# Kernel tuning notes

Hardware: AMD Instinct MI355X
Metric: run time of the kernel (lower is better)

Reference implementation:

```python
import jax, jax.numpy as jnp
import numpy as np

EMB = 1024
HEADS = 16
EPS = 1e-6


def setup_inputs() -> dict:
    key = jax.random.key(0)
    ks = jax.random.split(key, 12)
    B, S, D = 2, 2048, EMB
    scale = 1.0 / np.sqrt(D)
    inp = {
        "v": jax.random.normal(ks[0], (B, S, D), jnp.float32),
        "k": jax.random.normal(ks[1], (B, S, D), jnp.float32),
        "q": jax.random.normal(ks[2], (B, S, D), jnp.float32),
        "Wv": jax.random.normal(ks[3], (D, D), jnp.float32) * scale,
        "bv": jnp.zeros((D,), jnp.float32),
        "Wk": jax.random.normal(ks[4], (D, D), jnp.float32) * scale,
        "bk": jnp.zeros((D,), jnp.float32),
        "Wq": jax.random.normal(ks[5], (D, D), jnp.float32) * scale,
        "bq": jnp.zeros((D,), jnp.float32),
        "Wo": jax.random.normal(ks[6], (D, D), jnp.float32) * scale,
        "bo": jnp.zeros((D,), jnp.float32),
        "gamma": jnp.ones((D,), jnp.float32),
        "beta": jnp.zeros((D,), jnp.float32),
    }
    return inp


def reference(v, k, q, Wv, bv, Wk, bk, Wq, bq, Wo, bo, gamma, beta):
    B, S, D = q.shape
    H = HEADS
    d = D // H  # head depth

    def split_heads(x):  # [B,S,D] -> [B,H,S,d]
        return x.reshape(B, S, H, d).transpose(0, 2, 1, 3)

    V = split_heads(v @ Wv + bv)
    K = split_heads(k @ Wk + bk)
    Q = split_heads(q @ Wq + bq)

    # scaled dot-product attention (full score matrix, no mask)
    scores = jnp.einsum("bhqd,bhkd->bhqk", Q, K) / jnp.sqrt(jnp.float32(d))
    attn = jax.nn.softmax(scores, axis=-1)
    ctx = jnp.einsum("bhqk,bhkd->bhqd", attn, V)

    ctx = ctx.transpose(0, 2, 1, 3).reshape(B, S, D)
    out = ctx @ Wo + bo + q  # final dense + residual

    # LayerNormalization(epsilon=1e-6) over last axis
    mu = jnp.mean(out, axis=-1, keepdims=True)
    var = jnp.var(out, axis=-1, keepdims=True)
    return gamma * (out - mu) * jax.lax.rsqrt(var + EPS) + beta
```

## Files before the change

kernel.cpp:

```cpp
#include <hip/hip_runtime.h>
#include <hip/hip_bf16.h>
#include <math.h>

#define D_EMB 1024
#define NBATCH 2
#define SEQ 2048
#define NH 16
#define HDIM 64
#define MTOT (NBATCH*SEQ)
#define NT (SEQ/64)

typedef unsigned short u16;
typedef __attribute__((ext_vector_type(8))) short bf16x8;
typedef __attribute__((ext_vector_type(4))) float f32x4;
typedef __attribute__((ext_vector_type(16))) float f32x16;
typedef __attribute__((ext_vector_type(4))) unsigned short u16x4;
typedef __attribute__((ext_vector_type(4))) unsigned int u32x4;

__device__ __forceinline__ u16 f2b(float f) {
  union { float f; unsigned u; } x; x.f = f;
  unsigned r = x.u + 0x7fffu + ((x.u >> 16) & 1u);
  return (u16)(r >> 16);
}
__device__ __forceinline__ float b2f(u16 u) {
  union { unsigned u; float f; } x; x.u = ((unsigned)u) << 16;
  return x.f;
}

__device__ __forceinline__ void gld_lds16(const u16* g, u16* l) {
  __builtin_amdgcn_global_load_lds(
      (const __attribute__((address_space(1))) void*)g,
      (__attribute__((address_space(3))) void*)l, 16, 0, 0);
}

__global__ __launch_bounds__(256) void convert_qkv(
    const float* __restrict__ v, const float* __restrict__ k, const float* __restrict__ q,
    u16* __restrict__ vb, u16* __restrict__ kb, u16* __restrict__ qb) {
  int idx = blockIdx.x * 256 + threadIdx.x;
  float4 a;
  u16x4 o;
  a = ((const float4*)v)[idx];
  o.x = f2b(a.x); o.y = f2b(a.y); o.z = f2b(a.z); o.w = f2b(a.w);
  ((u16x4*)vb)[idx] = o;
  a = ((const float4*)k)[idx];
  o.x = f2b(a.x); o.y = f2b(a.y); o.z = f2b(a.z); o.w = f2b(a.w);
  ((u16x4*)kb)[idx] = o;
  a = ((const float4*)q)[idx];
  o.x = f2b(a.x); o.y = f2b(a.y); o.z = f2b(a.z); o.w = f2b(a.w);
  ((u16x4*)qb)[idx] = o;
}

__global__ __launch_bounds__(256) void transpose_w(
    const float* __restrict__ Wv, const float* __restrict__ Wk,
    const float* __restrict__ Wq, const float* __restrict__ Wo,
    u16* __restrict__ Wvt, u16* __restrict__ Wkt,
    u16* __restrict__ Wqt, u16* __restrict__ Wot) {
  __shared__ float tile[32][33];
  int z = blockIdx.z;
  const float* W = (z==0) ? Wv : (z==1) ? Wk : (z==2) ? Wq : Wo;
  u16* Wt = (z==0) ? Wvt : (z==1) ? Wkt : (z==2) ? Wqt : Wot;
  int tx = threadIdx.x, ty = threadIdx.y;
  int n0 = blockIdx.x * 32, k0 = blockIdx.y * 32;
#pragma unroll
  for (int i = 0; i < 4; ++i)
    tile[ty + i*8][tx] = W[(size_t)(k0 + ty + i*8) * D_EMB + n0 + tx];
  __syncthreads();
#pragma unroll
  for (int i = 0; i < 4; ++i)
    Wt[(size_t)(n0 + ty + i*8) * D_EMB + k0 + tx] = f2b(tile[tx][ty + i*8]);
}

__global__ __launch_bounds__(256) void transpose_v(
    const u16* __restrict__ Vh, u16* __restrict__ Vt) {
  __shared__ u16 t[64][65];
  const int bhx = blockIdx.y, s0 = blockIdx.x * 64;
  const int tid = threadIdx.x;
  const u16* src = Vh + ((size_t)bhx * SEQ + s0) * HDIM;
  const int r = tid >> 3, seg = (tid & 7) * 8;
  bf16x8 a0 = *(const bf16x8*)(src + (size_t)r * HDIM + seg);
  bf16x8 a1 = *(const bf16x8*)(src + (size_t)(r + 32) * HDIM + seg);
#pragma unroll
  for (int j = 0; j < 8; ++j) {
    t[r][seg + j] = (u16)a0[j];
    t[r + 32][seg + j] = (u16)a1[j];
  }
  __syncthreads();
  const int dd = tid >> 3, ss = (tid & 7) * 8;
  bf16x8 w0, w1;
#pragma unroll
  for (int j = 0; j < 8; ++j) {
    w0[j] = (short)t[ss + j][dd];
    w1[j] = (short)t[ss + j][dd + 32];
  }
  *(bf16x8*)(Vt + ((size_t)bhx * HDIM + dd) * SEQ + s0 + ss) = w0;
  *(bf16x8*)(Vt + ((size_t)bhx * HDIM + dd + 32) * SEQ + s0 + ss) = w1;
}

__device__ __forceinline__ void gemm_loop64(
    const u16* __restrict__ A, const u16* __restrict__ Bt,
    u16* lds_a, u16* lds_b, int bm, int bn, int wid, int lane,
    f32x4 acc[4][2]) {
#pragma unroll 1
  for (int kt = 0; kt < D_EMB/64; ++kt) {
    __syncthreads();
#pragma unroll
    for (int i = 0; i < 2; ++i) {
      int chunk = wid*2 + i;
      int row = chunk*8 + (lane >> 3);
      int slot = (lane & 7) ^ (row & 7);
      gld_lds16(A + (size_t)(bm*64 + row) * D_EMB + kt*64 + slot*8,
                lds_a + chunk*512);
    }
#pragma unroll
    for (int i = 0; i < 4; ++i) {
      int chunk = i*4 + wid;
      int row = chunk*8 + (lane >> 3);
      int slot = (lane & 7) ^ (row & 7);
      gld_lds16(Bt + (size_t)(bn*128 + row) * D_EMB + kt*64 + slot*8,
                lds_b + chunk*512);
    }
    __syncthreads();
#pragma unroll
    for (int st = 0; st < 2; ++st) {
      bf16x8 af[4], bfr[2];
#pragma unroll
      for (int mb = 0; mb < 4; ++mb) {
        int row = mb*16 + (lane & 15);
        int slot = (st*4 + (lane >> 4)) ^ (row & 7);
        af[mb] = *(const bf16x8*)(lds_a + row*64 + slot*8);
      }
#pragma unroll
      for (int nb = 0; nb < 2; ++nb) {
        int row = wid*32 + nb*16 + (lane & 15);
        int slot = (st*4 + (lane >> 4)) ^ (row & 7);
        bfr[nb] = *(const bf16x8*)(lds_b + row*64 + slot*8);
      }
#pragma unroll
      for (int mb = 0; mb < 4; ++mb)
#pragma unroll
        for (int nb = 0; nb < 2; ++nb)
          acc[mb][nb] = __builtin_amdgcn_mfma_f32_16x16x32_bf16(af[mb], bfr[nb], acc[mb][nb], 0, 0, 0);
    }
  }
}

__global__ __launch_bounds__(256) void gemm_qkv(
    const u16* __restrict__ vb, const u16* __restrict__ kb, const u16* __restrict__ qb,
    const u16* __restrict__ Wvt, const u16* __restrict__ Wkt, const u16* __restrict__ Wqt,
    const float* __restrict__ bv, const float* __restrict__ bk, const float* __restrict__ bq,
    u16* __restrict__ Vh, u16* __restrict__ Kh, u16* __restrict__ Qh) {
  __shared__ u16 lds_a[64*64];
  __shared__ u16 lds_b[128*64];
  int z = blockIdx.z;
  const u16* A  = (z==0) ? vb : (z==1) ? kb : qb;
  const u16* Bt = (z==0) ? Wvt : (z==1) ? Wkt : Wqt;
  const float* bias = (z==0) ? bv : (z==1) ? bk : bq;
  u16* Out = (z==0) ? Vh : (z==1) ? Kh : Qh;
  int tid = threadIdx.x, wid = tid >> 6, lane = tid & 63;
  int bm = blockIdx.y, bn = blockIdx.x;
  f32x4 acc[4][2];
#pragma unroll
  for (int i = 0; i < 4; ++i)
#pragma unroll
    for (int j = 0; j < 2; ++j) acc[i][j] = (f32x4){0.f,0.f,0.f,0.f};
  gemm_loop64(A, Bt, lds_a, lds_b, bm, bn, wid, lane, acc);
  int g = lane >> 4, c = lane & 15;
  const float scl = (z == 2) ? 0.18033688f : 1.0f;
#pragma unroll
  for (int mb = 0; mb < 4; ++mb) {
    int row0 = bm*64 + mb*16 + g*4;
#pragma unroll
    for (int nb = 0; nb < 2; ++nb) {
      int col = bn*128 + wid*32 + nb*16 + c;
      float bsv = bias[col];
      int h = col >> 6, dd = col & 63;
#pragma unroll
      for (int r = 0; r < 4; ++r) {
        int m = row0 + r; int b = m >> 11, s = m & (SEQ-1);
        Out[(((size_t)b*NH + h)*SEQ + s)*HDIM + dd] = f2b((acc[mb][nb][r] + bsv) * scl);
      }
    }
  }
}

__global__ __launch_bounds__(256, 2) void attn_k(
    const u16* __restrict__ Qh, const u16* __restrict__ Kh,
    const u16* __restrict__ Vt, u16* __restrict__ ctx) {
  __shared__ u16 kt_lds[2][64*64];
  __shared__ u16 vt_lds[2][64*64];
  const int tid = threadIdx.x, wid = tid >> 6, lane = tid & 63;
  const int lo5 = lane & 31, hi = lane >> 5;
  const int bid = blockIdx.x;
  const int xcd = bid & 7, idx = bid >> 3;
  const int qblk = idx & 15, bhg = idx >> 4;
  const int bh = bhg * 8 + xcd;
  const int qb = qblk * 128 + wid * 32;
  const size_t base = (size_t)bh * SEQ * HDIM;

  const int srow = tid >> 3;
  const int c0 = (tid & 7) ^ (srow & 7) ^ (srow >> 3);
  const int c1 = c0 ^ 4;
  const u16* kp0 = Kh + base + (size_t)srow * HDIM + c0*8;
  const u16* kp1 = Kh + base + (size_t)(srow+32) * HDIM + c1*8;
  const u16* vp0 = Vt + base + (size_t)srow * SEQ + c0*8;
  const u16* vp1 = Vt + base + (size_t)(srow+32) * SEQ + c1*8;

  const int r7 = lo5 & 7, r3 = lo5 >> 3;
  int offs0[4], offs1[4];
#pragma unroll
  for (int t = 0; t < 4; ++t) {
    int p = (2*t + hi) ^ r7 ^ r3;
    offs0[t] = lo5*128 + p*16;
    offs1[t] = (lo5+32)*128 + (p^4)*16;
  }
  const char* ktbase = (const char*)&kt_lds[0][0];
  const char* vtbase = (const char*)&vt_lds[0][0];

  bf16x8 qf[4];
#pragma unroll
  for (int t = 0; t < 4; ++t)
    qf[t] = *(const bf16x8*)(Qh + base + (size_t)(qb + lo5)*HDIM + t*16 + hi*8);

  f32x16 z16;
#pragma unroll
  for (int i = 0; i < 16; ++i) z16[i] = 0.f;

  f32x16 o0, o1;
#pragma unroll
  for (int i = 0; i < 16; ++i) { o0[i] = 0.f; o1[i] = 0.f; }
  float lsum = 0.f;

#define STAGE(B) do { \
    gld_lds16(kp0, &kt_lds[B][wid*512]); \
    gld_lds16(kp1, &kt_lds[B][2048 + wid*512]); \
    gld_lds16(vp0, &vt_lds[B][wid*512]); \
    gld_lds16(vp1, &vt_lds[B][2048 + wid*512]); \
    kp0 += 64*HDIM; kp1 += 64*HDIM; vp0 += 64; vp1 += 64; \
  } while (0)

#define TILE(B, VMSTR, DOSTAGE) do { \
    asm volatile("s_waitcnt " VMSTR ::: "memory"); \
    __builtin_amdgcn_sched_barrier(0); \
    __builtin_amdgcn_s_barrier();             \
    __builtin_amdgcn_sched_barrier(0); \
    const char* kb_ = ktbase + (B)*8192; \
    const char* vb_ = vtbase + (B)*8192; \
    bf16x8 kf0[4], kf1[4], vf0[4], vf1[4]; \
    _Pragma("unroll") for (int t = 0; t < 4; ++t) { \
      kf0[t] = *(const bf16x8*)(kb_ + offs0[t]); \
      kf1[t] = *(const bf16x8*)(kb_ + offs1[t]); \
      vf0[t] = *(const bf16x8*)(vb_ + offs0[t]); \
      vf1[t] = *(const bf16x8*)(vb_ + offs1[t]); } \
    asm volatile("s_waitcnt lgkmcnt(0)" ::: "memory"); \
    __builtin_amdgcn_sched_barrier(0); \
    __builtin_amdgcn_s_barrier();             \
    __builtin_amdgcn_sched_barrier(0); \
    if (DOSTAGE) { STAGE(B); } \
    __builtin_amdgcn_sched_barrier(0); \
    __builtin_amdgcn_s_setprio(1); \
    f32x16 st0 = __builtin_amdgcn_mfma_f32_32x32x16_bf16(kf0[0], qf[0], z16, 0, 0, 0); \
    f32x16 st1 = __builtin_amdgcn_mfma_f32_32x32x16_bf16(kf1[0], qf[0], z16, 0, 0, 0); \
    _Pragma("unroll") for (int t = 1; t < 4; ++t) { \
      st0 = __builtin_amdgcn_mfma_f32_32x32x16_bf16(kf0[t], qf[t], st0, 0, 0, 0); \
      st1 = __builtin_amdgcn_mfma_f32_32x32x16_bf16(kf1[t], qf[t], st1, 0, 0, 0); } \
    __builtin_amdgcn_s_setprio(0); \
    _Pragma("unroll") for (int r = 0; r < 16; ++r) { \
      st0[r] = exp2f(st0[r]); st1[r] = exp2f(st1[r]); } \
    float ps = st0[0] + st0[1]; \
    _Pragma("unroll") for (int r = 2; r < 16; ++r) ps += st0[r]; \
    _Pragma("unroll") for (int r = 0; r < 16; ++r) ps += st1[r]; \
    lsum += ps; \
    bf16x8 pa[4]; \
    _Pragma("unroll") for (int ks = 0; ks < 2; ++ks) { \
      const f32x16& s_ = ks ? st1 : st0; \
      unsigned X[8]; \
      _Pragma("unroll") for (int w = 0; w < 8; ++w) { \
        float lo_f = s_[2*w], hi_f = s_[2*w + 1]; \
        asm("v_cvt_pk_bf16_f32 %0, %1, %2" : "=v"(X[w]) : "v"(lo_f), "v"(hi_f)); } \
      asm volatile("v_permlane32_swap_b32 %0, %1" : "+v"(X[0]), "+v"(X[2])); \
      asm volatile("v_permlane32_swap_b32 %0, %1" : "+v"(X[1]), "+v"(X[3])); \
      asm volatile("v_permlane32_swap_b32 %0, %1" : "+v"(X[4]), "+v"(X[6])); \
      asm volatile("v_permlane32_swap_b32 %0, %1" : "+v"(X[5]), "+v"(X[7])); \
      union { u32x4 u; bf16x8 b; } cva, cvb; \
      cva.u = (u32x4){X[0], X[1], X[2], X[3]}; \
      cvb.u = (u32x4){X[4], X[5], X[6], X[7]}; \
      pa[2*ks]   = cva.b; \
      pa[2*ks+1] = cvb.b; } \
    __builtin_amdgcn_s_setprio(1); \
    _Pragma("unroll") for (int t = 0; t < 4; ++t) { \
      o0 = __builtin_amdgcn_mfma_f32_32x32x16_bf16(pa[t], vf0[t], o0, 0, 0, 0); \
      o1 = __builtin_amdgcn_mfma_f32_32x32x16_bf16(pa[t], vf1[t], o1, 0, 0, 0); } \
    __builtin_amdgcn_s_setprio(0); \
  } while (0)

  STAGE(0);
  STAGE(1);

#pragma unroll 1
  for (int kv = 0; kv < NT - 2; kv += 2) {
    TILE(0, "vmcnt(4)", 1);
    TILE(1, "vmcnt(4)", 1);
  }
  TILE(0, "vmcnt(4)", 0);
  TILE(1, "vmcnt(0)", 0);

#undef STAGE
#undef TILE

  lsum += __shfl_xor(lsum, 32);
  float linv = 1.0f / lsum;
  const int b = bh >> 4, h = bh & 15;
#pragma unroll
  for (int r = 0; r < 16; ++r) {
    int crow = (r & 3) + 8*(r >> 2) + 4*hi;
    float lr = __int_as_float(
        __builtin_amdgcn_ds_bpermute(crow << 2, __float_as_int(linv)));
    int s = qb + crow;
    u16* row = ctx + ((size_t)(b*SEQ + s))*D_EMB + h*64;
    row[lo5]      = f2b(o0[r] * lr);
    row[32 + lo5] = f2b(o1[r] * lr);
  }
}

__global__ __launch_bounds__(256) void gemm_out(
    const u16* __restrict__ ctx, const u16* __restrict__ Wot,
    const float* __restrict__ bo, const u16* __restrict__ resid,
    u16* __restrict__ preln) {
  __shared__ u16 lds_a[64*64];
  __shared__ u16 lds_b[128*64];
  int tid = threadIdx.x, wid = tid >> 6, lane = tid & 63;
  int bm = blockIdx.y, bn = blockIdx.x;
  f32x4 acc[4][2];
#pragma unroll
  for (int i = 0; i < 4; ++i)
#pragma unroll
    for (int j = 0; j < 2; ++j) acc[i][j] = (f32x4){0.f,0.f,0.f,0.f};
  gemm_loop64(ctx, Wot, lds_a, lds_b, bm, bn, wid, lane, acc);
  int g = lane >> 4, c = lane & 15;
#pragma unroll
  for (int mb = 0; mb < 4; ++mb) {
    int row0 = bm*64 + mb*16 + g*4;
#pragma unroll
    for (int nb = 0; nb < 2; ++nb) {
      int col = bn*128 + wid*32 + nb*16 + c;
      float bsv = bo[col];
#pragma unroll
      for (int r = 0; r < 4; ++r) {
        int m = row0 + r;
        float v = acc[mb][nb][r] + bsv + b2f(resid[(size_t)m*D_EMB + col]);
        preln[(size_t)m*D_EMB + col] = f2b(v);
      }
    }
  }
}

__global__ __launch_bounds__(256) void ln_k(
    const u16* __restrict__ preln, const float* __restrict__ gamma,
    const float* __restrict__ beta, float* __restrict__ out) {
  int row = blockIdx.x, tid = threadIdx.x;
  u16x4 xr = ((const u16x4*)(preln + (size_t)row*D_EMB))[tid];
  float x0 = b2f(xr.x), x1 = b2f(xr.y), x2 = b2f(xr.z), x3 = b2f(xr.w);
  float s  = x0 + x1 + x2 + x3;
  float ss = x0*x0 + x1*x1 + x2*x2 + x3*x3;
#pragma unroll
  for (int off = 32; off; off >>= 1) {
    s  += __shfl_xor(s, off);
    ss += __shfl_xor(ss, off);
  }
  __shared__ float red_s[4], red_ss[4];
  int wid = tid >> 6, lane = tid & 63;
  if (lane == 0) { red_s[wid] = s; red_ss[wid] = ss; }
  __syncthreads();
  s  = red_s[0] + red_s[1] + red_s[2] + red_s[3];
  ss = red_ss[0] + red_ss[1] + red_ss[2] + red_ss[3];
  float mu = s * (1.0f/1024.0f);
  float var = ss * (1.0f/1024.0f) - mu*mu;
  float rstd = rsqrtf(var + 1e-6f);
  float4 gm = ((const float4*)gamma)[tid];
  float4 bt = ((const float4*)beta)[tid];
  float4 y;
  y.x = (x0 - mu)*rstd*gm.x + bt.x;
  y.y = (x1 - mu)*rstd*gm.y + bt.y;
  y.z = (x2 - mu)*rstd*gm.z + bt.z;
  y.w = (x3 - mu)*rstd*gm.w + bt.w;
  ((float4*)(out + (size_t)row*D_EMB))[tid] = y;
}

extern "C" void kernel_launch(void* const* d_in, const int* in_sizes, int n_in,
                              void* d_out, int out_size, void* d_ws, size_t ws_size,
                              hipStream_t stream) {
  const float* v_in  = (const float*)d_in[0];
  const float* k_in  = (const float*)d_in[1];
  const float* q_in  = (const float*)d_in[2];
  const float* Wv    = (const float*)d_in[3];
  const float* bv    = (const float*)d_in[4];
  const float* Wk    = (const float*)d_in[5];
  const float* bk    = (const float*)d_in[6];
  const float* Wq    = (const float*)d_in[7];
  const float* bq    = (const float*)d_in[8];
  const float* Wo    = (const float*)d_in[9];
  const float* bo    = (const float*)d_in[10];
  const float* gamma = (const float*)d_in[11];
  const float* beta  = (const float*)d_in[12];
  char* ws = (char*)d_ws;

  const size_t TOKB = (size_t)MTOT * D_EMB * 2;
  const size_t WB   = (size_t)D_EMB * D_EMB * 2;
  size_t o_qb = 0;
  size_t o_kb = o_qb + TOKB;
  size_t o_vb = o_kb + TOKB;
  size_t o_wq = o_vb + TOKB;
  size_t o_wk = o_wq + WB;
  size_t o_wv = o_wk + WB;
  size_t o_wo = o_wv + WB;
  size_t o_Qh = o_wo + WB;
  size_t o_Kh = o_Qh + TOKB;
  size_t o_Vt = o_Kh + TOKB;
  size_t o_cx = o_Vt + TOKB;

  u16* qb  = (u16*)(ws + o_qb);
  u16* kb  = (u16*)(ws + o_kb);
  u16* vb  = (u16*)(ws + o_vb);
  u16* wqt = (u16*)(ws + o_wq);
  u16* wkt = (u16*)(ws + o_wk);
  u16* wvt = (u16*)(ws + o_wv);
  u16* wot = (u16*)(ws + o_wo);
  u16* Qh  = (u16*)(ws + o_Qh);
  u16* Kh  = (u16*)(ws + o_Kh);
  u16* Vt  = (u16*)(ws + o_Vt);
  u16* cx  = (u16*)(ws + o_cx);
  u16* Vh  = cx;
  u16* preln = vb;

  convert_qkv<<<4096, 256, 0, stream>>>(v_in, k_in, q_in, vb, kb, qb);
  transpose_w<<<dim3(32, 32, 4), dim3(32, 8), 0, stream>>>(Wv, Wk, Wq, Wo, wvt, wkt, wqt, wot);
  gemm_qkv<<<dim3(8, 64, 3), 256, 0, stream>>>(vb, kb, qb, wvt, wkt, wqt, bv, bk, bq, Vh, Kh, Qh);
  transpose_v<<<dim3(32, 32), 256, 0, stream>>>(Vh, Vt);
  attn_k<<<512, 256, 0, stream>>>(Qh, Kh, Vt, cx);
  gemm_out<<<dim3(8, 64), 256, 0, stream>>>(cx, wot, bo, qb, preln);
  ln_k<<<4096, 256, 0, stream>>>(preln, gamma, beta, (float*)d_out);
}
```

Measured before the change: 150.2 us.

## Fuse fp32→bf16 input conversion and V transpose into the QKV GEMM

```diff
diff --git a/kernel.cpp b/kernel.cpp
--- a/kernel.cpp
+++ b/kernel.cpp
@@ -11,6 +11,7 @@
 #define NT (SEQ/64)
 
 typedef unsigned short u16;
+typedef unsigned long long u64;
 typedef __attribute__((ext_vector_type(8))) short bf16x8;
 typedef __attribute__((ext_vector_type(4))) float f32x4;
 typedef __attribute__((ext_vector_type(16))) float f32x16;
@@ -31,23 +32,6 @@
   __builtin_amdgcn_global_load_lds(
       (const __attribute__((address_space(1))) void*)g,
       (__attribute__((address_space(3))) void*)l, 16, 0, 0);
-}
-
-__global__ __launch_bounds__(256) void convert_qkv(
-    const float* __restrict__ v, const float* __restrict__ k, const float* __restrict__ q,
-    u16* __restrict__ vb, u16* __restrict__ kb, u16* __restrict__ qb) {
-  int idx = blockIdx.x * 256 + threadIdx.x;
-  float4 a;
-  u16x4 o;
-  a = ((const float4*)v)[idx];
-  o.x = f2b(a.x); o.y = f2b(a.y); o.z = f2b(a.z); o.w = f2b(a.w);
-  ((u16x4*)vb)[idx] = o;
-  a = ((const float4*)k)[idx];
-  o.x = f2b(a.x); o.y = f2b(a.y); o.z = f2b(a.z); o.w = f2b(a.w);
-  ((u16x4*)kb)[idx] = o;
-  a = ((const float4*)q)[idx];
-  o.x = f2b(a.x); o.y = f2b(a.y); o.z = f2b(a.z); o.w = f2b(a.w);
-  ((u16x4*)qb)[idx] = o;
 }
 
 __global__ __launch_bounds__(256) void transpose_w(
@@ -70,34 +54,9 @@
     Wt[(size_t)(n0 + ty + i*8) * D_EMB + k0 + tx] = f2b(tile[tx][ty + i*8]);
 }
 
-__global__ __launch_bounds__(256) void transpose_v(
-    const u16* __restrict__ Vh, u16* __restrict__ Vt) {
-  __shared__ u16 t[64][65];
-  const int bhx = blockIdx.y, s0 = blockIdx.x * 64;
-  const int tid = threadIdx.x;
-  const u16* src = Vh + ((size_t)bhx * SEQ + s0) * HDIM;
-  const int r = tid >> 3, seg = (tid & 7) * 8;
-  bf16x8 a0 = *(const bf16x8*)(src + (size_t)r * HDIM + seg);
-  bf16x8 a1 = *(const bf16x8*)(src + (size_t)(r + 32) * HDIM + seg);
-#pragma unroll
-  for (int j = 0; j < 8; ++j) {
-    t[r][seg + j] = (u16)a0[j];
-    t[r + 32][seg + j] = (u16)a1[j];
-  }
-  __syncthreads();
-  const int dd = tid >> 3, ss = (tid & 7) * 8;
-  bf16x8 w0, w1;
-#pragma unroll
-  for (int j = 0; j < 8; ++j) {
-    w0[j] = (short)t[ss + j][dd];
-    w1[j] = (short)t[ss + j][dd + 32];
-  }
-  *(bf16x8*)(Vt + ((size_t)bhx * HDIM + dd) * SEQ + s0 + ss) = w0;
-  *(bf16x8*)(Vt + ((size_t)bhx * HDIM + dd + 32) * SEQ + s0 + ss) = w1;
-}
-
+template<bool F32A>
 __device__ __forceinline__ void gemm_loop64(
-    const u16* __restrict__ A, const u16* __restrict__ Bt,
+    const void* __restrict__ Av, const u16* __restrict__ Bt,
     u16* lds_a, u16* lds_b, int bm, int bn, int wid, int lane,
     f32x4 acc[4][2]) {
 #pragma unroll 1
@@ -108,8 +67,23 @@
       int chunk = wid*2 + i;
       int row = chunk*8 + (lane >> 3);
       int slot = (lane & 7) ^ (row & 7);
-      gld_lds16(A + (size_t)(bm*64 + row) * D_EMB + kt*64 + slot*8,
-                lds_a + chunk*512);
+      if constexpr (F32A) {
+        const float* Af = (const float*)Av +
+            (size_t)(bm*64 + row) * D_EMB + kt*64 + slot*8;
+        float4 fa = ((const float4*)Af)[0];
+        float4 fb = ((const float4*)Af)[1];
+        unsigned X0, X1, X2, X3;
+        asm("v_cvt_pk_bf16_f32 %0, %1, %2" : "=v"(X0) : "v"(fa.x), "v"(fa.y));
+        asm("v_cvt_pk_bf16_f32 %0, %1, %2" : "=v"(X1) : "v"(fa.z), "v"(fa.w));
+        asm("v_cvt_pk_bf16_f32 %0, %1, %2" : "=v"(X2) : "v"(fb.x), "v"(fb.y));
+        asm("v_cvt_pk_bf16_f32 %0, %1, %2" : "=v"(X3) : "v"(fb.z), "v"(fb.w));
+        union { u32x4 u; bf16x8 b; } cv;
+        cv.u = (u32x4){X0, X1, X2, X3};
+        *(bf16x8*)(lds_a + chunk*512 + lane*8) = cv.b;
+      } else {
+        gld_lds16((const u16*)Av + (size_t)(bm*64 + row) * D_EMB + kt*64 + slot*8,
+                  lds_a + chunk*512);
+      }
     }
 #pragma unroll
     for (int i = 0; i < 4; ++i) {
@@ -145,17 +119,20 @@
 }
 
 __global__ __launch_bounds__(256) void gemm_qkv(
-    const u16* __restrict__ vb, const u16* __restrict__ kb, const u16* __restrict__ qb,
-    const u16* __restrict__ Wvt, const u16* __restrict__ Wkt, const u16* __restrict__ Wqt,
-    const float* __restrict__ bv, const float* __restrict__ bk, const float* __restrict__ bq,
-    u16* __restrict__ Vh, u16* __restrict__ Kh, u16* __restrict__ Qh) {
-  __shared__ u16 lds_a[64*64];
-  __shared__ u16 lds_b[128*64];
+    const float* __restrict__ v_in, const float* __restrict__ k_in,
+    const float* __restrict__ q_in,
+    const u16* __restrict__ Wvt, const u16* __restrict__ Wkt,
+    const u16* __restrict__ Wqt,
+    const float* __restrict__ bv, const float* __restrict__ bk,
+    const float* __restrict__ bq,
+    u16* __restrict__ Vt, u16* __restrict__ Kh, u16* __restrict__ Qh) {
+  __shared__ u16 smem[64*64 + 128*64];
+  u16* lds_a = smem;
+  u16* lds_b = smem + 64*64;
   int z = blockIdx.z;
-  const u16* A  = (z==0) ? vb : (z==1) ? kb : qb;
-  const u16* Bt = (z==0) ? Wvt : (z==1) ? Wkt : Wqt;
+  const float* A = (z==0) ? v_in : (z==1) ? k_in : q_in;
+  const u16* Bt  = (z==0) ? Wvt : (z==1) ? Wkt : Wqt;
   const float* bias = (z==0) ? bv : (z==1) ? bk : bq;
-  u16* Out = (z==0) ? Vh : (z==1) ? Kh : Qh;
   int tid = threadIdx.x, wid = tid >> 6, lane = tid & 63;
   int bm = blockIdx.y, bn = blockIdx.x;
   f32x4 acc[4][2];
@@ -163,21 +140,47 @@
   for (int i = 0; i < 4; ++i)
 #pragma unroll
     for (int j = 0; j < 2; ++j) acc[i][j] = (f32x4){0.f,0.f,0.f,0.f};
-  gemm_loop64(A, Bt, lds_a, lds_b, bm, bn, wid, lane, acc);
+  gemm_loop64<true>(A, Bt, lds_a, lds_b, bm, bn, wid, lane, acc);
   int g = lane >> 4, c = lane & 15;
-  const float scl = (z == 2) ? 0.18033688f : 1.0f;
-#pragma unroll
-  for (int mb = 0; mb < 4; ++mb) {
-    int row0 = bm*64 + mb*16 + g*4;
-#pragma unroll
-    for (int nb = 0; nb < 2; ++nb) {
-      int col = bn*128 + wid*32 + nb*16 + c;
-      float bsv = bias[col];
-      int h = col >> 6, dd = col & 63;
-#pragma unroll
-      for (int r = 0; r < 4; ++r) {
-        int m = row0 + r; int b = m >> 11, s = m & (SEQ-1);
-        Out[(((size_t)b*NH + h)*SEQ + s)*HDIM + dd] = f2b((acc[mb][nb][r] + bsv) * scl);
+  if (z == 0) {
+    __syncthreads();
+    u16* vt_tile = smem;
+#pragma unroll
+    for (int mb = 0; mb < 4; ++mb) {
+#pragma unroll
+      for (int nb = 0; nb < 2; ++nb) {
+        int col_l = wid*32 + nb*16 + c;
+        float bsv = bias[bn*128 + col_l];
+        union { u64 u; u16 a[4]; } w;
+#pragma unroll
+        for (int r = 0; r < 4; ++r) w.a[r] = f2b(acc[mb][nb][r] + bsv);
+        *(u64*)(vt_tile + col_l*68 + mb*16 + g*4) = w.u;
+      }
+    }
+    __syncthreads();
+    const int dd_row = tid >> 1, half = tid & 1;
+    const int h = bn*2 + (dd_row >> 6), dd = dd_row & 63;
+    const int b = bm >> 5, sbase = (bm & 31) * 64;
+    const u16* srcl = vt_tile + dd_row*68 + half*32;
+    u16* dst = Vt + (((size_t)b*NH + h)*HDIM + dd)*SEQ + sbase + half*32;
+#pragma unroll
+    for (int j = 0; j < 8; ++j) ((u64*)dst)[j] = ((const u64*)srcl)[j];
+  } else {
+    u16* Out = (z==1) ? Kh : Qh;
+    const float scl = (z == 2) ? 0.18033688f : 1.0f;
+#pragma unroll
+    for (int mb = 0; mb < 4; ++mb) {
+      int row0 = bm*64 + mb*16 + g*4;
+#pragma unroll
+      for (int nb = 0; nb < 2; ++nb) {
+        int col = bn*128 + wid*32 + nb*16 + c;
+        float bsv = bias[col];
+        int h = col >> 6, dd = col & 63;
+#pragma unroll
+        for (int r = 0; r < 4; ++r) {
+          int m = row0 + r; int b = m >> 11, s = m & (SEQ-1);
+          Out[(((size_t)b*NH + h)*SEQ + s)*HDIM + dd] = f2b((acc[mb][nb][r] + bsv) * scl);
+        }
       }
     }
   }
@@ -324,10 +327,11 @@
 
 __global__ __launch_bounds__(256) void gemm_out(
     const u16* __restrict__ ctx, const u16* __restrict__ Wot,
-    const float* __restrict__ bo, const u16* __restrict__ resid,
+    const float* __restrict__ bo, const float* __restrict__ resid,
     u16* __restrict__ preln) {
-  __shared__ u16 lds_a[64*64];
-  __shared__ u16 lds_b[128*64];
+  __shared__ u16 smem[64*64 + 128*64];
+  u16* lds_a = smem;
+  u16* lds_b = smem + 64*64;
   int tid = threadIdx.x, wid = tid >> 6, lane = tid & 63;
   int bm = blockIdx.y, bn = blockIdx.x;
   f32x4 acc[4][2];
@@ -335,7 +339,7 @@
   for (int i = 0; i < 4; ++i)
 #pragma unroll
     for (int j = 0; j < 2; ++j) acc[i][j] = (f32x4){0.f,0.f,0.f,0.f};
-  gemm_loop64(ctx, Wot, lds_a, lds_b, bm, bn, wid, lane, acc);
+  gemm_loop64<false>(ctx, Wot, lds_a, lds_b, bm, bn, wid, lane, acc);
   int g = lane >> 4, c = lane & 15;
 #pragma unroll
   for (int mb = 0; mb < 4; ++mb) {
@@ -347,7 +351,7 @@
 #pragma unroll
       for (int r = 0; r < 4; ++r) {
         int m = row0 + r;
-        float v = acc[mb][nb][r] + bsv + b2f(resid[(size_t)m*D_EMB + col]);
+        float v = acc[mb][nb][r] + bsv + resid[(size_t)m*D_EMB + col];
         preln[(size_t)m*D_EMB + col] = f2b(v);
       }
     }
@@ -406,10 +410,8 @@
 
   const size_t TOKB = (size_t)MTOT * D_EMB * 2;
   const size_t WB   = (size_t)D_EMB * D_EMB * 2;
-  size_t o_qb = 0;
-  size_t o_kb = o_qb + TOKB;
-  size_t o_vb = o_kb + TOKB;
-  size_t o_wq = o_vb + TOKB;
+  size_t o_pl = 0;
+  size_t o_wq = o_pl + 3*TOKB;
   size_t o_wk = o_wq + WB;
   size_t o_wv = o_wk + WB;
   size_t o_wo = o_wv + WB;
@@ -418,9 +420,7 @@
   size_t o_Vt = o_Kh + TOKB;
   size_t o_cx = o_Vt + TOKB;
 
-  u16* qb  = (u16*)(ws + o_qb);
-  u16* kb  = (u16*)(ws + o_kb);
-  u16* vb  = (u16*)(ws + o_vb);
+  u16* preln = (u16*)(ws + o_pl);
   u16* wqt = (u16*)(ws + o_wq);
   u16* wkt = (u16*)(ws + o_wk);
   u16* wvt = (u16*)(ws + o_wv);
@@ -429,14 +429,10 @@
   u16* Kh  = (u16*)(ws + o_Kh);
   u16* Vt  = (u16*)(ws + o_Vt);
   u16* cx  = (u16*)(ws + o_cx);
-  u16* Vh  = cx;
-  u16* preln = vb;
-
-  convert_qkv<<<4096, 256, 0, stream>>>(v_in, k_in, q_in, vb, kb, qb);
+
   transpose_w<<<dim3(32, 32, 4), dim3(32, 8), 0, stream>>>(Wv, Wk, Wq, Wo, wvt, wkt, wqt, wot);
-  gemm_qkv<<<dim3(8, 64, 3), 256, 0, stream>>>(vb, kb, qb, wvt, wkt, wqt, bv, bk, bq, Vh, Kh, Qh);
-  transpose_v<<<dim3(32, 32), 256, 0, stream>>>(Vh, Vt);
+  gemm_qkv<<<dim3(8, 64, 3), 256, 0, stream>>>(v_in, k_in, q_in, wvt, wkt, wqt, bv, bk, bq, Vt, Kh, Qh);
   attn_k<<<512, 256, 0, stream>>>(Qh, Kh, Vt, cx);
-  gemm_out<<<dim3(8, 64), 256, 0, stream>>>(cx, wot, bo, qb, preln);
+  gemm_out<<<dim3(8, 64), 256, 0, stream>>>(cx, wot, bo, q_in, preln);
   ln_k<<<4096, 256, 0, stream>>>(preln, gamma, beta, (float*)d_out);
 }
```

After: 158.3 us. 5.4% more time.

## Fuse V transpose into QKV GEMM epilogue and remap blocks for XCD locality

Applied to the files above, without the earlier changes.

```diff
diff --git a/kernel.cpp b/kernel.cpp
--- a/kernel.cpp
+++ b/kernel.cpp
@@ -11,6 +11,7 @@
 #define NT (SEQ/64)
 
 typedef unsigned short u16;
+typedef unsigned long long u64;
 typedef __attribute__((ext_vector_type(8))) short bf16x8;
 typedef __attribute__((ext_vector_type(4))) float f32x4;
 typedef __attribute__((ext_vector_type(16))) float f32x16;
@@ -70,32 +71,6 @@
     Wt[(size_t)(n0 + ty + i*8) * D_EMB + k0 + tx] = f2b(tile[tx][ty + i*8]);
 }
 
-__global__ __launch_bounds__(256) void transpose_v(
-    const u16* __restrict__ Vh, u16* __restrict__ Vt) {
-  __shared__ u16 t[64][65];
-  const int bhx = blockIdx.y, s0 = blockIdx.x * 64;
-  const int tid = threadIdx.x;
-  const u16* src = Vh + ((size_t)bhx * SEQ + s0) * HDIM;
-  const int r = tid >> 3, seg = (tid & 7) * 8;
-  bf16x8 a0 = *(const bf16x8*)(src + (size_t)r * HDIM + seg);
-  bf16x8 a1 = *(const bf16x8*)(src + (size_t)(r + 32) * HDIM + seg);
-#pragma unroll
-  for (int j = 0; j < 8; ++j) {
-    t[r][seg + j] = (u16)a0[j];
-    t[r + 32][seg + j] = (u16)a1[j];
-  }
-  __syncthreads();
-  const int dd = tid >> 3, ss = (tid & 7) * 8;
-  bf16x8 w0, w1;
-#pragma unroll
-  for (int j = 0; j < 8; ++j) {
-    w0[j] = (short)t[ss + j][dd];
-    w1[j] = (short)t[ss + j][dd + 32];
-  }
-  *(bf16x8*)(Vt + ((size_t)bhx * HDIM + dd) * SEQ + s0 + ss) = w0;
-  *(bf16x8*)(Vt + ((size_t)bhx * HDIM + dd + 32) * SEQ + s0 + ss) = w1;
-}
-
 __device__ __forceinline__ void gemm_loop64(
     const u16* __restrict__ A, const u16* __restrict__ Bt,
     u16* lds_a, u16* lds_b, int bm, int bn, int wid, int lane,
@@ -148,16 +123,18 @@
     const u16* __restrict__ vb, const u16* __restrict__ kb, const u16* __restrict__ qb,
     const u16* __restrict__ Wvt, const u16* __restrict__ Wkt, const u16* __restrict__ Wqt,
     const float* __restrict__ bv, const float* __restrict__ bk, const float* __restrict__ bq,
-    u16* __restrict__ Vh, u16* __restrict__ Kh, u16* __restrict__ Qh) {
-  __shared__ u16 lds_a[64*64];
-  __shared__ u16 lds_b[128*64];
-  int z = blockIdx.z;
+    u16* __restrict__ Vt, u16* __restrict__ Kh, u16* __restrict__ Qh) {
+  __shared__ u16 smem[64*64 + 128*64];
+  u16* lds_a = smem;
+  u16* lds_b = smem + 64*64;
+  const int bid = blockIdx.x;
+  const int x = bid & 7, t = bid >> 3;
+  const int bn = t & 7, t2 = t >> 3;
+  const int bm = (t2 & 7)*8 + x, z = t2 >> 3;
   const u16* A  = (z==0) ? vb : (z==1) ? kb : qb;
   const u16* Bt = (z==0) ? Wvt : (z==1) ? Wkt : Wqt;
   const float* bias = (z==0) ? bv : (z==1) ? bk : bq;
-  u16* Out = (z==0) ? Vh : (z==1) ? Kh : Qh;
   int tid = threadIdx.x, wid = tid >> 6, lane = tid & 63;
-  int bm = blockIdx.y, bn = blockIdx.x;
   f32x4 acc[4][2];
 #pragma unroll
   for (int i = 0; i < 4; ++i)
@@ -165,19 +142,45 @@
     for (int j = 0; j < 2; ++j) acc[i][j] = (f32x4){0.f,0.f,0.f,0.f};
   gemm_loop64(A, Bt, lds_a, lds_b, bm, bn, wid, lane, acc);
   int g = lane >> 4, c = lane & 15;
-  const float scl = (z == 2) ? 0.18033688f : 1.0f;
-#pragma unroll
-  for (int mb = 0; mb < 4; ++mb) {
-    int row0 = bm*64 + mb*16 + g*4;
-#pragma unroll
-    for (int nb = 0; nb < 2; ++nb) {
-      int col = bn*128 + wid*32 + nb*16 + c;
-      float bsv = bias[col];
-      int h = col >> 6, dd = col & 63;
-#pragma unroll
-      for (int r = 0; r < 4; ++r) {
-        int m = row0 + r; int b = m >> 11, s = m & (SEQ-1);
-        Out[(((size_t)b*NH + h)*SEQ + s)*HDIM + dd] = f2b((acc[mb][nb][r] + bsv) * scl);
+  if (z == 0) {
+    __syncthreads();
+    u16* vt_tile = smem;
+#pragma unroll
+    for (int mb = 0; mb < 4; ++mb) {
+#pragma unroll
+      for (int nb = 0; nb < 2; ++nb) {
+        int col_l = wid*32 + nb*16 + c;
+        float bsv = bias[bn*128 + col_l];
+        union { u64 u; u16 a[4]; } w;
+#pragma unroll
+        for (int r = 0; r < 4; ++r) w.a[r] = f2b(acc[mb][nb][r] + bsv);
+        *(u64*)(vt_tile + col_l*68 + mb*16 + g*4) = w.u;
+      }
+    }
+    __syncthreads();
+    const int dd_row = tid >> 1, half = tid & 1;
+    const int h = bn*2 + (dd_row >> 6), dd = dd_row & 63;
+    const int b = bm >> 5, sbase = (bm & 31) * 64;
+    const u16* srcl = vt_tile + dd_row*68 + half*32;
+    u16* dst = Vt + (((size_t)b*NH + h)*HDIM + dd)*SEQ + sbase + half*32;
+#pragma unroll
+    for (int j = 0; j < 8; ++j) ((u64*)dst)[j] = ((const u64*)srcl)[j];
+  } else {
+    u16* Out = (z==1) ? Kh : Qh;
+    const float scl = (z == 2) ? 0.18033688f : 1.0f;
+#pragma unroll
+    for (int mb = 0; mb < 4; ++mb) {
+      int row0 = bm*64 + mb*16 + g*4;
+#pragma unroll
+      for (int nb = 0; nb < 2; ++nb) {
+        int col = bn*128 + wid*32 + nb*16 + c;
+        float bsv = bias[col];
+        int h = col >> 6, dd = col & 63;
+#pragma unroll
+        for (int r = 0; r < 4; ++r) {
+          int m = row0 + r; int b = m >> 11, s = m & (SEQ-1);
+          Out[(((size_t)b*NH + h)*SEQ + s)*HDIM + dd] = f2b((acc[mb][nb][r] + bsv) * scl);
+        }
       }
     }
   }
@@ -326,10 +329,13 @@
     const u16* __restrict__ ctx, const u16* __restrict__ Wot,
     const float* __restrict__ bo, const u16* __restrict__ resid,
     u16* __restrict__ preln) {
-  __shared__ u16 lds_a[64*64];
-  __shared__ u16 lds_b[128*64];
+  __shared__ u16 smem[64*64 + 128*64];
+  u16* lds_a = smem;
+  u16* lds_b = smem + 64*64;
+  const int bid = blockIdx.x;
+  const int x = bid & 7, t = bid >> 3;
+  const int bn = t & 7, bm = (t >> 3)*8 + x;
   int tid = threadIdx.x, wid = tid >> 6, lane = tid & 63;
-  int bm = blockIdx.y, bn = blockIdx.x;
   f32x4 acc[4][2];
 #pragma unroll
   for (int i = 0; i < 4; ++i)
@@ -429,14 +435,12 @@
   u16* Kh  = (u16*)(ws + o_Kh);
   u16* Vt  = (u16*)(ws + o_Vt);
   u16* cx  = (u16*)(ws + o_cx);
-  u16* Vh  = cx;
   u16* preln = vb;
 
   convert_qkv<<<4096, 256, 0, stream>>>(v_in, k_in, q_in, vb, kb, qb);
   transpose_w<<<dim3(32, 32, 4), dim3(32, 8), 0, stream>>>(Wv, Wk, Wq, Wo, wvt, wkt, wqt, wot);
-  gemm_qkv<<<dim3(8, 64, 3), 256, 0, stream>>>(vb, kb, qb, wvt, wkt, wqt, bv, bk, bq, Vh, Kh, Qh);
-  transpose_v<<<dim3(32, 32), 256, 0, stream>>>(Vh, Vt);
+  gemm_qkv<<<1536, 256, 0, stream>>>(vb, kb, qb, wvt, wkt, wqt, bv, bk, bq, Vt, Kh, Qh);
   attn_k<<<512, 256, 0, stream>>>(Qh, Kh, Vt, cx);
-  gemm_out<<<dim3(8, 64), 256, 0, stream>>>(cx, wot, bo, qb, preln);
+  gemm_out<<<512, 256, 0, stream>>>(cx, wot, bo, qb, preln);
   ln_k<<<4096, 256, 0, stream>>>(preln, gamma, beta, (float*)d_out);
 }
```

After: 137.7 us, median of 2. 1.09x faster.
